# Optimization experiments

Hardware: AMD Instinct MI355X
Metric: run time of the kernel (lower is better)

## Reference

```python
import jax, jax.numpy as jnp
import numpy as np

N_NODES = 100000
N_EDGES = 800000
ANNOT = 92
HID = 64
N_STEPS = 8
N_IDX = 20000


def setup_inputs() -> dict:
    key = jax.random.key(0)
    ks = jax.random.split(key, 12)
    s = 1.0 / np.sqrt(HID)
    return {
        'x': jax.random.normal(ks[0], (N_NODES, ANNOT), dtype=jnp.float32),
        'edge_index': jax.random.randint(ks[1], (2, N_EDGES), 0, N_NODES, dtype=jnp.int64),
        'idx': jax.random.randint(ks[2], (N_IDX,), 0, N_NODES, dtype=jnp.int64),
        'W_red': jax.random.normal(ks[3], (ANNOT, HID), dtype=jnp.float32) / np.sqrt(ANNOT),
        'b_red': jnp.zeros((HID,), dtype=jnp.float32),
        'W_g': jax.random.normal(ks[4], (N_STEPS, HID, HID), dtype=jnp.float32) * s,
        'w_ih': jax.random.normal(ks[5], (3 * HID, HID), dtype=jnp.float32) * s,
        'w_hh': jax.random.normal(ks[6], (3 * HID, HID), dtype=jnp.float32) * s,
        'b_ih': jax.random.normal(ks[7], (3 * HID,), dtype=jnp.float32) * s,
        'b_hh': jax.random.normal(ks[8], (3 * HID,), dtype=jnp.float32) * s,
        'W_lin': jax.random.normal(ks[9], (HID, 1), dtype=jnp.float32) * s,
        'b_lin': jnp.zeros((1,), dtype=jnp.float32),
    }


def _gru_cell(a, h, w_ih, w_hh, b_ih, b_hh):
    # a: aggregated messages [N, H]; h: hidden state [N, H]
    gi = a @ w_ih.T + b_ih  # [N, 3H]
    gh = h @ w_hh.T + b_hh
    i_r, i_z, i_n = jnp.split(gi, 3, axis=-1)
    h_r, h_z, h_n = jnp.split(gh, 3, axis=-1)
    r = jax.nn.sigmoid(i_r + h_r)
    z = jax.nn.sigmoid(i_z + h_z)
    n = jnp.tanh(i_n + r * h_n)
    return (1.0 - z) * n + z * h


def reference(x, edge_index, idx, W_red, b_red, W_g, w_ih, w_hh, b_ih, b_hh, W_lin, b_lin):
    src, dst = edge_index[0], edge_index[1]
    h = x @ W_red + b_red  # [N, H]

    def step(h, Wt):
        m = h @ Wt                                  # [N, H] per-step transform
        msg = jnp.take(m, src, axis=0)              # gather along edges [E, H]
        aggr = jax.ops.segment_sum(msg, dst, num_segments=N_NODES)  # scatter-add
        h_new = _gru_cell(aggr, h, w_ih, w_hh, b_ih, b_hh)
        return h_new, None

    h, _ = jax.lax.scan(step, h, W_g)
    sel = jnp.take(h, idx, axis=0)                  # index_select [B, H]
    return jax.nn.sigmoid(sel @ W_lin + b_lin)      # [B, 1]
```

## Files before the change

### kernel.cpp

```cpp
#include <hip/hip_runtime.h>
#include <hip/hip_bf16.h>

#define NN 100000
#define HH 64
#define AN 92
#define NSTEP 8
#define NGRP 6250
#define RB 768
#define CAP 64

typedef float f4v __attribute__((ext_vector_type(4)));
typedef short s8v __attribute__((ext_vector_type(8)));

__device__ __forceinline__ float sigf(float x) { return 1.0f / (1.0f + __expf(-x)); }
__device__ __forceinline__ float tanhfast(float x) { return 1.0f - 2.0f / (1.0f + __expf(2.0f * x)); }

__device__ __forceinline__ unsigned short tobf(float x) {
    __hip_bfloat16 b = __float2bfloat16(x);
    return __builtin_bit_cast(unsigned short, b);
}
__device__ __forceinline__ float frombf(unsigned short u) {
    return __int_as_float(((unsigned)u) << 16);
}

__device__ __forceinline__ int packpos(int k, int r) {
    int T = r >> 4, kh = k >> 5;
    int lane = ((k >> 3) & 3) * 16 + (r & 15);
    int j = k & 7;
    return ((T * 2 + kh) * 64 + lane) * 8 + j;
}

__global__ __launch_bounds__(256) void k_wcp(const float* __restrict__ Wg,
                                             const float* __restrict__ w_ih,
                                             const float* __restrict__ w_hh,
                                             unsigned short* __restrict__ Wcp,
                                             unsigned short* __restrict__ Whp) {
    __shared__ float wl[192 * 65];
    int wb = blockIdx.x;
    if (wb < 384) {
        for (int i = threadIdx.x; i < 192 * 64; i += 256) {
            int r = i >> 6, q = i & 63;
            wl[r * 65 + q] = w_ih[i];
        }
        __syncthreads();
        int gid = wb * 256 + threadIdx.x;
        int r = gid % 192;
        int k = (gid / 192) & 63;
        int t = gid / (192 * 64);
        const float* wg = Wg + t * 4096 + k * 64;
        float acc = 0.f;
#pragma unroll
        for (int q = 0; q < 64; ++q) acc = fmaf(wg[q], wl[r * 65 + q], acc);
        Wcp[t * 12288 + packpos(k, r)] = tobf(acc);
    } else {
        int gid = (wb - 384) * 256 + threadIdx.x;
        if (gid >= 192 * 64) return;
        int r = gid >> 6, k = gid & 63;
        Whp[packpos(k, r)] = tobf(w_hh[r * 64 + k]);
    }
}

__global__ __launch_bounds__(256) void k_plred(const int* __restrict__ src,
                                               const int* __restrict__ dst,
                                               int* __restrict__ cnt,
                                               int* __restrict__ srt, int E,
                                               const float* __restrict__ x,
                                               const float* __restrict__ W,
                                               const float* __restrict__ b,
                                               unsigned short* __restrict__ hb) {
    __shared__ __align__(16) unsigned short wrp[6144];
    __shared__ __align__(16) float xs[4][1472];
    int tid = threadIdx.x;
    if (blockIdx.x >= RB) {
        int e = (blockIdx.x - RB) * 256 + tid;
        if (e < E) {
            int d = dst[e];
            int pos = atomicAdd(cnt + d, 1);
            if (pos < CAP) srt[d * CAP + pos] = src[e];
        }
        return;
    }
    for (int i = tid; i < 96 * 64; i += 256) {
        int k = i >> 6, r = i & 63;
        float val = (k < AN) ? W[k * HH + r] : 0.f;
        int T = r >> 4, kh = k >> 5;
        int ln = ((k >> 3) & 3) * 16 + (r & 15);
        int j = k & 7;
        wrp[((T * 3 + kh) * 64 + ln) * 8 + j] = tobf(val);
    }
    __syncthreads();
    const s8v* wB = (const s8v*)wrp;
    int lane = tid & 63, wave = tid >> 6;
    int row16 = lane & 15, quad = lane >> 4;
    float bj[4];
#pragma unroll
    for (int t = 0; t < 4; ++t) bj[t] = b[t * 16 + row16];
    float4* xd = (float4*)xs[wave];
    const float* xrow = xs[wave] + row16 * AN;

    for (int g = blockIdx.x * 4 + wave; g < NGRP; g += RB * 4) {
        int n0 = g * 16;
        const float4* xsrc = (const float4*)(x + (size_t)n0 * AN);
#pragma unroll
        for (int i = 0; i < 5; ++i) xd[i * 64 + lane] = xsrc[i * 64 + lane];
        if (lane < 48) xd[320 + lane] = xsrc[320 + lane];
        s8v A[3];
#pragma unroll
        for (int kh = 0; kh < 3; ++kh) {
            int k0 = quad * 8 + kh * 32;
            float4 lo = *(const float4*)(xrow + k0);
            float4 hi;
            if (kh == 2 && quad == 3) hi = make_float4(0.f, 0.f, 0.f, 0.f);
            else hi = *(const float4*)(xrow + k0 + 4);
            s8v f;
            f[0] = (short)tobf(lo.x); f[1] = (short)tobf(lo.y);
            f[2] = (short)tobf(lo.z); f[3] = (short)tobf(lo.w);
            f[4] = (short)tobf(hi.x); f[5] = (short)tobf(hi.y);
            f[6] = (short)tobf(hi.z); f[7] = (short)tobf(hi.w);
            A[kh] = f;
        }
#pragma unroll
        for (int t = 0; t < 4; ++t) {
            f4v acc = {bj[t], bj[t], bj[t], bj[t]};
#pragma unroll
            for (int kh = 0; kh < 3; ++kh)
                acc = __builtin_amdgcn_mfma_f32_16x16x32_bf16(A[kh], wB[(t * 3 + kh) * 64 + lane], acc, 0, 0, 0);
#pragma unroll
            for (int reg = 0; reg < 4; ++reg) {
                int node = n0 + quad * 4 + reg;
                hb[(size_t)node * HH + t * 16 + row16] = tobf(acc[reg]);
            }
        }
    }
}

__global__ __launch_bounds__(256) void k_aggr(const unsigned short* __restrict__ hb,
                                              const int* __restrict__ cnt,
                                              const int* __restrict__ srt,
                                              unsigned short* __restrict__ Sb) {
    int gid = blockIdx.x * 256 + threadIdx.x;
    int wid = gid >> 6;
    int lane = threadIdx.x & 63;
    int half = lane >> 5;
    int ci = lane & 31;
    int n = wid * 2 + half;
    if (n >= NN) return;
    int st = n * CAP;
    int en = st + min(cnt[n], CAP);
    float aa[8], bb[8];
#pragma unroll
    for (int i = 0; i < 8; ++i) { aa[i] = 0.f; bb[i] = 0.f; }
    for (int j = st; j < en; j += 8) {
        unsigned u[8];
#pragma unroll
        for (int i = 0; i < 8; ++i) {
            int jj = j + i;
            int sidx = srt[min(jj, en - 1)];
            unsigned uu = *(const unsigned*)(hb + (size_t)sidx * HH + ci * 2);
            u[i] = (jj < en) ? uu : 0u;
        }
#pragma unroll
        for (int i = 0; i < 8; ++i) {
            aa[i] += frombf((unsigned short)u[i]);
            bb[i] += frombf((unsigned short)(u[i] >> 16));
        }
    }
    float A = ((aa[0] + aa[1]) + (aa[2] + aa[3])) + ((aa[4] + aa[5]) + (aa[6] + aa[7]));
    float B = ((bb[0] + bb[1]) + (bb[2] + bb[3])) + ((bb[4] + bb[5]) + (bb[6] + bb[7]));
    unsigned o = (unsigned)tobf(A) | ((unsigned)tobf(B) << 16);
    *(unsigned*)(Sb + (size_t)n * HH + ci * 2) = o;
}

__global__ __launch_bounds__(256) void k_gru(const unsigned short* __restrict__ Sb,
                                             unsigned short* __restrict__ hb,
                                             const unsigned short* __restrict__ Wcp_t,
                                             const unsigned short* __restrict__ Whp,
                                             const float* __restrict__ b_ih,
                                             const float* __restrict__ b_hh) {
    const s8v* wiB = (const s8v*)Wcp_t;
    const s8v* whB = (const s8v*)Whp;

    int lane = threadIdx.x & 63;
    int wave = threadIdx.x >> 6;
    int quad = lane >> 4, nidx = lane & 15;
    int g = blockIdx.x * 4 + wave;
    if (g >= NGRP) return;

    float brz[4], bzz[4], bin[4], bhn[4];
#pragma unroll
    for (int t = 0; t < 4; ++t) {
        int c = t * 16 + nidx;
        brz[t] = b_ih[c] + b_hh[c];
        bzz[t] = b_ih[64 + c] + b_hh[64 + c];
        bin[t] = b_ih[128 + c];
        bhn[t] = b_hh[128 + c];
    }

    int n0 = g * 16;
    size_t rowoff = (size_t)(n0 + nidx) * HH + quad * 8;
    s8v aS0 = *(const s8v*)(Sb + rowoff);
    s8v aS1 = *(const s8v*)(Sb + rowoff + 32);
    s8v aH0 = *(const s8v*)(hb + rowoff);
    s8v aH1 = *(const s8v*)(hb + rowoff + 32);

#pragma unroll
    for (int t = 0; t < 4; ++t) {
        f4v aRZ0 = {brz[t], brz[t], brz[t], brz[t]};
        f4v aRZ1 = {bzz[t], bzz[t], bzz[t], bzz[t]};
        f4v aIN  = {bin[t], bin[t], bin[t], bin[t]};
        f4v aHN  = {bhn[t], bhn[t], bhn[t], bhn[t]};
        aRZ0 = __builtin_amdgcn_mfma_f32_16x16x32_bf16(aS0, wiB[(t * 2 + 0) * 64 + lane], aRZ0, 0, 0, 0);
        aRZ0 = __builtin_amdgcn_mfma_f32_16x16x32_bf16(aS1, wiB[(t * 2 + 1) * 64 + lane], aRZ0, 0, 0, 0);
        aRZ0 = __builtin_amdgcn_mfma_f32_16x16x32_bf16(aH0, whB[(t * 2 + 0) * 64 + lane], aRZ0, 0, 0, 0);
        aRZ0 = __builtin_amdgcn_mfma_f32_16x16x32_bf16(aH1, whB[(t * 2 + 1) * 64 + lane], aRZ0, 0, 0, 0);
        int tz = t + 4;
        aRZ1 = __builtin_amdgcn_mfma_f32_16x16x32_bf16(aS0, wiB[(tz * 2 + 0) * 64 + lane], aRZ1, 0, 0, 0);
        aRZ1 = __builtin_amdgcn_mfma_f32_16x16x32_bf16(aS1, wiB[(tz * 2 + 1) * 64 + lane], aRZ1, 0, 0, 0);
        aRZ1 = __builtin_amdgcn_mfma_f32_16x16x32_bf16(aH0, whB[(tz * 2 + 0) * 64 + lane], aRZ1, 0, 0, 0);
        aRZ1 = __builtin_amdgcn_mfma_f32_16x16x32_bf16(aH1, whB[(tz * 2 + 1) * 64 + lane], aRZ1, 0, 0, 0);
        int tn = t + 8;
        aIN = __builtin_amdgcn_mfma_f32_16x16x32_bf16(aS0, wiB[(tn * 2 + 0) * 64 + lane], aIN, 0, 0, 0);
        aIN = __builtin_amdgcn_mfma_f32_16x16x32_bf16(aS1, wiB[(tn * 2 + 1) * 64 + lane], aIN, 0, 0, 0);
        aHN = __builtin_amdgcn_mfma_f32_16x16x32_bf16(aH0, whB[(tn * 2 + 0) * 64 + lane], aHN, 0, 0, 0);
        aHN = __builtin_amdgcn_mfma_f32_16x16x32_bf16(aH1, whB[(tn * 2 + 1) * 64 + lane], aHN, 0, 0, 0);
        int c = t * 16 + nidx;
#pragma unroll
        for (int reg = 0; reg < 4; ++reg) {
            int node = n0 + quad * 4 + reg;
            float rv = sigf(aRZ0[reg]);
            float zv = sigf(aRZ1[reg]);
            float nv = tanhfast(fmaf(rv, aHN[reg], aIN[reg]));
            size_t off = (size_t)node * HH + c;
            float ho = frombf(hb[off]);
            float hnew = fmaf(zv, ho - nv, nv);
            hb[off] = tobf(hnew);
        }
    }
}

__global__ __launch_bounds__(256) void k_readout(const unsigned short* __restrict__ hb,
                                                 const int* __restrict__ idx,
                                                 const float* __restrict__ Wl,
                                                 const float* __restrict__ bl,
                                                 float* __restrict__ out, int B) {
    int gid = blockIdx.x * 256 + threadIdx.x;
    int i = gid >> 6, lane = gid & 63;
    if (i >= B) return;
    int n = idx[i];
    float v = frombf(hb[(size_t)n * HH + lane]) * Wl[lane];
#pragma unroll
    for (int off = 32; off > 0; off >>= 1) v += __shfl_xor(v, off, 64);
    if (lane == 0) out[i] = sigf(v + bl[0]);
}

extern "C" void kernel_launch(void* const* d_in, const int* in_sizes, int n_in,
                              void* d_out, int out_size, void* d_ws, size_t ws_size,
                              hipStream_t stream) {
    const float* x     = (const float*)d_in[0];
    const int*   ei    = (const int*)d_in[1];
    const int*   idx   = (const int*)d_in[2];
    const float* W_red = (const float*)d_in[3];
    const float* b_red = (const float*)d_in[4];
    const float* W_g   = (const float*)d_in[5];
    const float* w_ih  = (const float*)d_in[6];
    const float* w_hh  = (const float*)d_in[7];
    const float* b_ih  = (const float*)d_in[8];
    const float* b_hh  = (const float*)d_in[9];
    const float* W_lin = (const float*)d_in[10];
    const float* b_lin = (const float*)d_in[11];
    float* out = (float*)d_out;
    const int E = in_sizes[1] / 2;
    const int B = in_sizes[2];
    const int* src = ei;
    const int* dst = ei + E;
    const int PB = (E + 255) / 256;

    unsigned short* hb  = (unsigned short*)d_ws;
    unsigned short* Sb  = hb + (size_t)NN * HH;
    unsigned short* Wcp = Sb + (size_t)NN * HH;
    unsigned short* Whp = Wcp + (size_t)NSTEP * 12288;
    int*            cnt = (int*)(Whp + 12288);
    int*            srt = cnt + NN;

    hipMemsetAsync(cnt, 0, NN * sizeof(int), stream);
    k_wcp<<<384 + 48, 256, 0, stream>>>(W_g, w_ih, w_hh, Wcp, Whp);

    k_plred<<<RB + PB, 256, 0, stream>>>(src, dst, cnt, srt, E,
                                         x, W_red, b_red, hb);

    for (int t = 0; t < NSTEP; ++t) {
        k_aggr<<<(NN / 2 * 64 + 255) / 256, 256, 0, stream>>>(hb, cnt, srt, Sb);
        k_gru<<<1563, 256, 0, stream>>>(Sb, hb, Wcp + (size_t)t * 12288, Whp,
                                        b_ih, b_hh);
    }

    k_readout<<<(B * 64 + 255) / 256, 256, 0, stream>>>(hb, idx, W_lin, b_lin, out, B);
}
```

Before: 501.1 us.

## Fuse aggregation and GRU into one per-step kernel with ping-pong hidden buffers

Merges the gather/sum aggregation kernel and the GRU MFMA kernel into a single 512-thread block per 16 nodes. The aggregated messages go through swizzled shared memory instead of a global Sb buffer, and the hidden state is double-buffered so the fused kernel can read old h while writing new h. This removes one launch per step and the global write and read of the aggregate. In exchange, four of the eight waves sit idle during the GRU phase, and each block now waits at a barrier on its slowest aggregation wave. After 8 steps the final state ends up in hb0, which the readout uses.

```diff
diff --git a/kernel.cpp b/kernel.cpp
--- a/kernel.cpp
+++ b/kernel.cpp
@@ -134,107 +134,100 @@
     }
 }
 
-__global__ __launch_bounds__(256) void k_aggr(const unsigned short* __restrict__ hb,
+__global__ __launch_bounds__(512) void k_step(const unsigned short* __restrict__ hbo,
+                                              unsigned short* __restrict__ hbn,
                                               const int* __restrict__ cnt,
                                               const int* __restrict__ srt,
-                                              unsigned short* __restrict__ Sb) {
-    int gid = blockIdx.x * 256 + threadIdx.x;
-    int wid = gid >> 6;
-    int lane = threadIdx.x & 63;
-    int half = lane >> 5;
-    int ci = lane & 31;
-    int n = wid * 2 + half;
-    if (n >= NN) return;
-    int st = n * CAP;
-    int en = st + min(cnt[n], CAP);
-    float aa[8], bb[8];
-#pragma unroll
-    for (int i = 0; i < 8; ++i) { aa[i] = 0.f; bb[i] = 0.f; }
-    for (int j = st; j < en; j += 8) {
-        unsigned u[8];
-#pragma unroll
-        for (int i = 0; i < 8; ++i) {
-            int jj = j + i;
-            int sidx = srt[min(jj, en - 1)];
-            unsigned uu = *(const unsigned*)(hb + (size_t)sidx * HH + ci * 2);
-            u[i] = (jj < en) ? uu : 0u;
-        }
-#pragma unroll
-        for (int i = 0; i < 8; ++i) {
-            aa[i] += frombf((unsigned short)u[i]);
-            bb[i] += frombf((unsigned short)(u[i] >> 16));
-        }
-    }
-    float A = ((aa[0] + aa[1]) + (aa[2] + aa[3])) + ((aa[4] + aa[5]) + (aa[6] + aa[7]));
-    float B = ((bb[0] + bb[1]) + (bb[2] + bb[3])) + ((bb[4] + bb[5]) + (bb[6] + bb[7]));
-    unsigned o = (unsigned)tobf(A) | ((unsigned)tobf(B) << 16);
-    *(unsigned*)(Sb + (size_t)n * HH + ci * 2) = o;
-}
-
-__global__ __launch_bounds__(256) void k_gru(const unsigned short* __restrict__ Sb,
-                                             unsigned short* __restrict__ hb,
-                                             const unsigned short* __restrict__ Wcp_t,
-                                             const unsigned short* __restrict__ Whp,
-                                             const float* __restrict__ b_ih,
-                                             const float* __restrict__ b_hh) {
+                                              const unsigned short* __restrict__ Wcp_t,
+                                              const unsigned short* __restrict__ Whp,
+                                              const float* __restrict__ b_ih,
+                                              const float* __restrict__ b_hh) {
+    __shared__ __align__(16) unsigned char sb[2048];
+    int tid = threadIdx.x;
+    int lane = tid & 63, wave = tid >> 6;
+    int n0 = blockIdx.x * 16;
+
+    {
+        int half = lane >> 5;
+        int ci = lane & 31;
+        int n = n0 + wave * 2 + half;
+        int st = n * CAP;
+        int en = st + min(cnt[n], CAP);
+        float aa[8], bb[8];
+#pragma unroll
+        for (int i = 0; i < 8; ++i) { aa[i] = 0.f; bb[i] = 0.f; }
+        for (int j = st; j < en; j += 8) {
+            unsigned u[8];
+#pragma unroll
+            for (int i = 0; i < 8; ++i) {
+                int jj = j + i;
+                int sidx = srt[min(jj, en - 1)];
+                unsigned uu = *(const unsigned*)(hbo + (size_t)sidx * HH + ci * 2);
+                u[i] = (jj < en) ? uu : 0u;
+            }
+#pragma unroll
+            for (int i = 0; i < 8; ++i) {
+                aa[i] += frombf((unsigned short)u[i]);
+                bb[i] += frombf((unsigned short)(u[i] >> 16));
+            }
+        }
+        float A = ((aa[0] + aa[1]) + (aa[2] + aa[3])) + ((aa[4] + aa[5]) + (aa[6] + aa[7]));
+        float B = ((bb[0] + bb[1]) + (bb[2] + bb[3])) + ((bb[4] + bb[5]) + (bb[6] + bb[7]));
+        unsigned o = (unsigned)tobf(A) | ((unsigned)tobf(B) << 16);
+        int row = wave * 2 + half;
+        int cb = (row * 128 + ci * 4) ^ ((row & 7) << 4);
+        *(unsigned*)(&sb[cb]) = o;
+    }
+    __syncthreads();
+    if (wave >= 4) return;
+
     const s8v* wiB = (const s8v*)Wcp_t;
     const s8v* whB = (const s8v*)Whp;
-
-    int lane = threadIdx.x & 63;
-    int wave = threadIdx.x >> 6;
     int quad = lane >> 4, nidx = lane & 15;
-    int g = blockIdx.x * 4 + wave;
-    if (g >= NGRP) return;
-
-    float brz[4], bzz[4], bin[4], bhn[4];
-#pragma unroll
-    for (int t = 0; t < 4; ++t) {
-        int c = t * 16 + nidx;
-        brz[t] = b_ih[c] + b_hh[c];
-        bzz[t] = b_ih[64 + c] + b_hh[64 + c];
-        bin[t] = b_ih[128 + c];
-        bhn[t] = b_hh[128 + c];
-    }
-
-    int n0 = g * 16;
+    int t = wave;
+    int c = t * 16 + nidx;
+    float brz = b_ih[c] + b_hh[c];
+    float bzz = b_ih[64 + c] + b_hh[64 + c];
+    float bin = b_ih[128 + c];
+    float bhn = b_hh[128 + c];
+
+    int rb0 = (nidx * 128 + quad * 16) ^ ((nidx & 7) << 4);
+    int rb1 = (nidx * 128 + 64 + quad * 16) ^ ((nidx & 7) << 4);
+    s8v aS0 = *(const s8v*)(&sb[rb0]);
+    s8v aS1 = *(const s8v*)(&sb[rb1]);
     size_t rowoff = (size_t)(n0 + nidx) * HH + quad * 8;
-    s8v aS0 = *(const s8v*)(Sb + rowoff);
-    s8v aS1 = *(const s8v*)(Sb + rowoff + 32);
-    s8v aH0 = *(const s8v*)(hb + rowoff);
-    s8v aH1 = *(const s8v*)(hb + rowoff + 32);
-
-#pragma unroll
-    for (int t = 0; t < 4; ++t) {
-        f4v aRZ0 = {brz[t], brz[t], brz[t], brz[t]};
-        f4v aRZ1 = {bzz[t], bzz[t], bzz[t], bzz[t]};
-        f4v aIN  = {bin[t], bin[t], bin[t], bin[t]};
-        f4v aHN  = {bhn[t], bhn[t], bhn[t], bhn[t]};
-        aRZ0 = __builtin_amdgcn_mfma_f32_16x16x32_bf16(aS0, wiB[(t * 2 + 0) * 64 + lane], aRZ0, 0, 0, 0);
-        aRZ0 = __builtin_amdgcn_mfma_f32_16x16x32_bf16(aS1, wiB[(t * 2 + 1) * 64 + lane], aRZ0, 0, 0, 0);
-        aRZ0 = __builtin_amdgcn_mfma_f32_16x16x32_bf16(aH0, whB[(t * 2 + 0) * 64 + lane], aRZ0, 0, 0, 0);
-        aRZ0 = __builtin_amdgcn_mfma_f32_16x16x32_bf16(aH1, whB[(t * 2 + 1) * 64 + lane], aRZ0, 0, 0, 0);
-        int tz = t + 4;
-        aRZ1 = __builtin_amdgcn_mfma_f32_16x16x32_bf16(aS0, wiB[(tz * 2 + 0) * 64 + lane], aRZ1, 0, 0, 0);
-        aRZ1 = __builtin_amdgcn_mfma_f32_16x16x32_bf16(aS1, wiB[(tz * 2 + 1) * 64 + lane], aRZ1, 0, 0, 0);
-        aRZ1 = __builtin_amdgcn_mfma_f32_16x16x32_bf16(aH0, whB[(tz * 2 + 0) * 64 + lane], aRZ1, 0, 0, 0);
-        aRZ1 = __builtin_amdgcn_mfma_f32_16x16x32_bf16(aH1, whB[(tz * 2 + 1) * 64 + lane], aRZ1, 0, 0, 0);
-        int tn = t + 8;
-        aIN = __builtin_amdgcn_mfma_f32_16x16x32_bf16(aS0, wiB[(tn * 2 + 0) * 64 + lane], aIN, 0, 0, 0);
-        aIN = __builtin_amdgcn_mfma_f32_16x16x32_bf16(aS1, wiB[(tn * 2 + 1) * 64 + lane], aIN, 0, 0, 0);
-        aHN = __builtin_amdgcn_mfma_f32_16x16x32_bf16(aH0, whB[(tn * 2 + 0) * 64 + lane], aHN, 0, 0, 0);
-        aHN = __builtin_amdgcn_mfma_f32_16x16x32_bf16(aH1, whB[(tn * 2 + 1) * 64 + lane], aHN, 0, 0, 0);
-        int c = t * 16 + nidx;
-#pragma unroll
-        for (int reg = 0; reg < 4; ++reg) {
-            int node = n0 + quad * 4 + reg;
-            float rv = sigf(aRZ0[reg]);
-            float zv = sigf(aRZ1[reg]);
-            float nv = tanhfast(fmaf(rv, aHN[reg], aIN[reg]));
-            size_t off = (size_t)node * HH + c;
-            float ho = frombf(hb[off]);
-            float hnew = fmaf(zv, ho - nv, nv);
-            hb[off] = tobf(hnew);
-        }
+    s8v aH0 = *(const s8v*)(hbo + rowoff);
+    s8v aH1 = *(const s8v*)(hbo + rowoff + 32);
+
+    f4v aRZ0 = {brz, brz, brz, brz};
+    f4v aRZ1 = {bzz, bzz, bzz, bzz};
+    f4v aIN  = {bin, bin, bin, bin};
+    f4v aHN  = {bhn, bhn, bhn, bhn};
+    aRZ0 = __builtin_amdgcn_mfma_f32_16x16x32_bf16(aS0, wiB[(t * 2 + 0) * 64 + lane], aRZ0, 0, 0, 0);
+    aRZ0 = __builtin_amdgcn_mfma_f32_16x16x32_bf16(aS1, wiB[(t * 2 + 1) * 64 + lane], aRZ0, 0, 0, 0);
+    aRZ0 = __builtin_amdgcn_mfma_f32_16x16x32_bf16(aH0, whB[(t * 2 + 0) * 64 + lane], aRZ0, 0, 0, 0);
+    aRZ0 = __builtin_amdgcn_mfma_f32_16x16x32_bf16(aH1, whB[(t * 2 + 1) * 64 + lane], aRZ0, 0, 0, 0);
+    int tz = t + 4;
+    aRZ1 = __builtin_amdgcn_mfma_f32_16x16x32_bf16(aS0, wiB[(tz * 2 + 0) * 64 + lane], aRZ1, 0, 0, 0);
+    aRZ1 = __builtin_amdgcn_mfma_f32_16x16x32_bf16(aS1, wiB[(tz * 2 + 1) * 64 + lane], aRZ1, 0, 0, 0);
+    aRZ1 = __builtin_amdgcn_mfma_f32_16x16x32_bf16(aH0, whB[(tz * 2 + 0) * 64 + lane], aRZ1, 0, 0, 0);
+    aRZ1 = __builtin_amdgcn_mfma_f32_16x16x32_bf16(aH1, whB[(tz * 2 + 1) * 64 + lane], aRZ1, 0, 0, 0);
+    int tn = t + 8;
+    aIN = __builtin_amdgcn_mfma_f32_16x16x32_bf16(aS0, wiB[(tn * 2 + 0) * 64 + lane], aIN, 0, 0, 0);
+    aIN = __builtin_amdgcn_mfma_f32_16x16x32_bf16(aS1, wiB[(tn * 2 + 1) * 64 + lane], aIN, 0, 0, 0);
+    aHN = __builtin_amdgcn_mfma_f32_16x16x32_bf16(aH0, whB[(tn * 2 + 0) * 64 + lane], aHN, 0, 0, 0);
+    aHN = __builtin_amdgcn_mfma_f32_16x16x32_bf16(aH1, whB[(tn * 2 + 1) * 64 + lane], aHN, 0, 0, 0);
+
+#pragma unroll
+    for (int reg = 0; reg < 4; ++reg) {
+        int node = n0 + quad * 4 + reg;
+        float rv = sigf(aRZ0[reg]);
+        float zv = sigf(aRZ1[reg]);
+        float nv = tanhfast(fmaf(rv, aHN[reg], aIN[reg]));
+        size_t off = (size_t)node * HH + c;
+        float ho = frombf(hbo[off]);
+        float hnew = fmaf(zv, ho - nv, nv);
+        hbn[off] = tobf(hnew);
     }
 }
 
@@ -275,24 +268,26 @@
     const int* dst = ei + E;
     const int PB = (E + 255) / 256;
 
-    unsigned short* hb  = (unsigned short*)d_ws;
-    unsigned short* Sb  = hb + (size_t)NN * HH;
-    unsigned short* Wcp = Sb + (size_t)NN * HH;
+    unsigned short* hb0 = (unsigned short*)d_ws;
+    unsigned short* hb1 = hb0 + (size_t)NN * HH;
+    unsigned short* Wcp = hb1 + (size_t)NN * HH;
     unsigned short* Whp = Wcp + (size_t)NSTEP * 12288;
     int*            cnt = (int*)(Whp + 12288);
     int*            srt = cnt + NN;
+    unsigned short* hbb[2] = {hb0, hb1};
 
     hipMemsetAsync(cnt, 0, NN * sizeof(int), stream);
     k_wcp<<<384 + 48, 256, 0, stream>>>(W_g, w_ih, w_hh, Wcp, Whp);
 
     k_plred<<<RB + PB, 256, 0, stream>>>(src, dst, cnt, srt, E,
-                                         x, W_red, b_red, hb);
+                                         x, W_red, b_red, hb0);
 
     for (int t = 0; t < NSTEP; ++t) {
-        k_aggr<<<(NN / 2 * 64 + 255) / 256, 256, 0, stream>>>(hb, cnt, srt, Sb);
-        k_gru<<<1563, 256, 0, stream>>>(Sb, hb, Wcp + (size_t)t * 12288, Whp,
-                                        b_ih, b_hh);
-    }
-
-    k_readout<<<(B * 64 + 255) / 256, 256, 0, stream>>>(hb, idx, W_lin, b_lin, out, B);
-}
+        k_step<<<NGRP, 512, 0, stream>>>(hbb[t & 1], hbb[(t + 1) & 1],
+                                         cnt, srt,
+                                         Wcp + (size_t)t * 12288, Whp,
+                                         b_ih, b_hh);
+    }
+
+    k_readout<<<(B * 64 + 255) / 256, 256, 0, stream>>>(hb0, idx, W_lin, b_lin, out, B);
+}
```

Result: faster. 476.1 us (-5.0%).
